# Optimization experiments

Hardware: AMD Instinct MI355X
Metric: run time of the kernel (lower is better)

The kernel has to match this reference:

```python
import jax, jax.numpy as jnp
import numpy as np

EDGES = np.array([[0,13],[0,1],[0,4],[0,10],[0,7],[13,14],[14,15],[15,16],[1,2],[2,3],
                  [3,17],[4,5],[5,6],[6,18],[10,11],[11,12],[12,19],[7,8],[8,9],[9,20]])
N = 21
EPS = 1e-5


def _build_adj():
    # adj_mx_from_edges: symmetric binary adjacency + self-loops, row-normalized (D^-1 (A+I))
    A = np.zeros((N, N), np.float32)
    A[EDGES[:, 0], EDGES[:, 1]] = 1.0
    A = np.maximum(A, A.T)
    A = A + np.eye(N, dtype=np.float32)
    A = A / A.sum(1, keepdims=True)
    return A


def setup_inputs() -> dict:
    key = jax.random.key(0)
    ks = jax.random.split(key, 10)
    B, C, H, W = 64, 256, 64, 64
    s = 0.05
    return {
        "feature_s": jax.random.normal(ks[0], (B, C, H, W), jnp.float32),
        "target_s": jax.random.uniform(ks[1], (B, N, H, W), jnp.float32),
        "adj": jnp.asarray(_build_adj()),
        "bn_gamma": jnp.ones((N,), jnp.float32),
        "bn_beta": jnp.zeros((N,), jnp.float32),
        "gru_wx": s * jax.random.normal(ks[2], (256, 768), jnp.float32),
        "gru_wh": s * jax.random.normal(ks[3], (256, 768), jnp.float32),
        "gru_bx": jnp.zeros((768,), jnp.float32),
        "gru_bh": jnp.zeros((768,), jnp.float32),
        "w_g1": s * jax.random.normal(ks[4], (2, 256, 256), jnp.float32),
        "b_g1": jnp.zeros((256,), jnp.float32),
        "w_g2": s * jax.random.normal(ks[5], (2, 256, 256), jnp.float32),
        "b_g2": jnp.zeros((256,), jnp.float32),
        "w_out": s * jax.random.normal(ks[6], (2, 256, 3), jnp.float32),
        "b_out": jnp.zeros((3,), jnp.float32),
    }


def _batchnorm1d(x, gamma, beta):
    # x: [B, 21, C]; BatchNorm1d over channel dim 21 (stats over batch and length)
    mean = jnp.mean(x, axis=(0, 2), keepdims=True)
    var = jnp.var(x, axis=(0, 2), keepdims=True)
    xn = (x - mean) * jax.lax.rsqrt(var + EPS)
    return xn * gamma[None, :, None] + beta[None, :, None]


def _gru(x, wx, wh, bx, bh):
    # standard GRU scanned over the 21-joint axis; x: [B, N, 256] -> [B, N, 256]
    B, n, Hd = x.shape
    xg = jnp.einsum('bnc,ch->bnh', x, wx) + bx  # [B, N, 3H]

    def step(h, xg_t):
        hg = h @ wh + bh
        r = jax.nn.sigmoid(xg_t[..., :Hd] + hg[..., :Hd])
        z = jax.nn.sigmoid(xg_t[..., Hd:2 * Hd] + hg[..., Hd:2 * Hd])
        ncand = jnp.tanh(xg_t[..., 2 * Hd:] + r * hg[..., 2 * Hd:])
        h_new = (1.0 - z) * ncand + z * h
        return h_new, h_new

    h0 = jnp.zeros((B, Hd), x.dtype)
    _, ys = jax.lax.scan(step, h0, jnp.swapaxes(xg, 0, 1))
    return jnp.swapaxes(ys, 0, 1)


def _laplacian(adj):
    # normalized Laplacian L = I - D^{-1/2} A D^{-1/2}
    d = adj.sum(-1)
    dinv = jnp.where(d > 0, jax.lax.rsqrt(jnp.where(d > 0, d, 1.0)), 0.0)
    return jnp.eye(N, dtype=adj.dtype) - dinv[:, None] * adj * dinv[None, :]


def _chebconv(x, L, w, b):
    # K=2 Chebyshev conv: T0 = I, T1 = L ->  x @ W0 + (L x) @ W1 + b
    return jnp.einsum('bnc,co->bno', x, w[0]) + jnp.einsum('nm,bmc,co->bno', L, x, w[1]) + b


def reference(feature_s, target_s, adj, bn_gamma, bn_beta,
              gru_wx, gru_wh, gru_bx, gru_bh,
              w_g1, b_g1, w_g2, b_g2, w_out, b_out):
    B, C, H, W = feature_s.shape
    # batched correlation: [B, 21, HW] x [B, HW, C] -> [B, 21, C]
    q = jnp.einsum('bjp,bcp->bjc',
                   target_s.reshape(B, N, H * W),
                   feature_s.reshape(B, C, H * W))
    q = _batchnorm1d(q, bn_gamma, bn_beta)
    q = jnp.where(q > 0, q, 0.1 * q)  # LeakyReLU(0.1)
    q = _gru(q, gru_wx, gru_wh, gru_bx, gru_bh)
    # _ResChebGC: two graph convs with ReLU + residual (dropout = identity in eval)
    L = _laplacian(adj)
    h = jax.nn.relu(_chebconv(q, L, w_g1, b_g1))
    h = jax.nn.relu(_chebconv(h, L, w_g2, b_g2))
    x = q + h
    return _chebconv(x, L, w_out, b_out)  # [B, 21, 3]
```

## Files before the change

### kernel.cpp

```cpp
#include <hip/hip_runtime.h>
#include <cstdint>

#define B   64
#define NJ  21
#define CHN 256
#define HW  4096
#define G3  768

typedef _Float16 f16x8 __attribute__((ext_vector_type(8)));
typedef float    f32x4 __attribute__((ext_vector_type(4)));
typedef _Float16 f16x2 __attribute__((ext_vector_type(2)));
typedef __fp16   fp16x2v __attribute__((ext_vector_type(2)));
union PKU { fp16x2v h; unsigned u; };
union HU { unsigned u; f16x2 h; };

static __device__ inline unsigned pack_f16(float a, float b){
  HU u; u.h.x = (_Float16)a; u.h.y = (_Float16)b; return u.u;
}

static __device__ inline float fdot2f(unsigned wu, unsigned hu, float acc){
  HU w, h; w.u = wu; h.u = hu;
#if __has_builtin(__builtin_amdgcn_fdot2)
  return __builtin_amdgcn_fdot2(w.h, h.h, acc, false);
#else
  return acc + (float)w.h.x*(float)h.h.x + (float)w.h.y*(float)h.h.y;
#endif
}

__global__ __launch_bounds__(64) void k_lap(const float* __restrict__ adj, float* __restrict__ L){
  __shared__ float dinv[NJ];
  int t = threadIdx.x;
  if (t < NJ){
    float s = 0.f;
    for (int j=0;j<NJ;j++) s += adj[t*NJ+j];
    dinv[t] = s > 0.f ? 1.f/sqrtf(s) : 0.f;
  }
  __syncthreads();
  for (int idx=t; idx<NJ*NJ; idx+=64){
    int i = idx/NJ, j = idx%NJ;
    L[idx] = (i==j ? 1.f : 0.f) - dinv[i]*adj[idx]*dinv[j];
  }
}

__global__ __launch_bounds__(256,4) void k_corr3(const float* __restrict__ T,
    const float* __restrict__ F, _Float16* __restrict__ P){
  int bid = blockIdx.x;
  int nb = bid & 3, b = (bid>>2)&63, kb = bid>>8;
  int t = threadIdx.x;
  int w = t>>6, l = t&63;
  __shared__ __align__(16) unsigned short At[2][32*64];
  __shared__ __align__(16) unsigned short Bt[2][64*64];

  for (int i=t; i<704; i+=256){
    int bi = (i>=352) ? 1 : 0; int r2 = i - bi*352;
    int r = 21 + (r2>>5); int kk = r2 & 31;
    *(unsigned*)((char*)&At[bi][0] + r*128 + kk*4) = 0u;
  }

  bool isF = (t < 128);
  bool isT = (t >= 128) && (t < 170);
  const float4* gp = nullptr; int srow = 0, shalf = 0;
  if (isF){
    srow = t>>1; shalf = t&1;
    gp = (const float4*)(F + ((size_t)b*CHN + nb*64 + srow)*HW + (size_t)kb*1024) + shalf*8;
  } else if (isT){
    int tt = t-128; srow = tt>>1; shalf = tt&1;
    gp = (const float4*)(T + ((size_t)b*NJ + srow)*HW + (size_t)kb*1024) + shalf*8;
  }
  float4 ld[8];
  if (gp){
    #pragma unroll
    for (int i=0;i<8;i++) ld[i] = gp[i];
  }

  f32x4 acc0 = {0.f,0.f,0.f,0.f}, acc1 = {0.f,0.f,0.f,0.f};
  int arow0 = (l&15);
  int brow  = w*16 + (l&15);
  int kbyt  = (l>>4)*16;

  for (int s=0; s<16; ++s){
    int bi = s & 1;
    if (gp){
      unsigned short* tile = isF ? &Bt[bi][0] : &At[bi][0];
      #pragma unroll
      for (int q=0;q<4;q++){
        PKU p0, p1, p2, p3;
        p0.h = __builtin_amdgcn_cvt_pkrtz(ld[2*q].x,   ld[2*q].y);
        p1.h = __builtin_amdgcn_cvt_pkrtz(ld[2*q].z,   ld[2*q].w);
        p2.h = __builtin_amdgcn_cvt_pkrtz(ld[2*q+1].x, ld[2*q+1].y);
        p3.h = __builtin_amdgcn_cvt_pkrtz(ld[2*q+1].z, ld[2*q+1].w);
        int addr = (srow*128 + shalf*64 + q*16) ^ ((srow&7)<<4);
        uint4 v; v.x = p0.u; v.y = p1.u; v.z = p2.u; v.w = p3.u;
        *(uint4*)((char*)tile + addr) = v;
      }
      if (s < 15){
        const float4* gn = gp + (size_t)(s+1)*16;
        #pragma unroll
        for (int i=0;i<8;i++) ld[i] = gn[i];
      }
    }
    asm volatile("s_waitcnt lgkmcnt(0)\n\ts_barrier" ::: "memory");
    #pragma unroll
    for (int kc=0;kc<2;kc++){
      int kb2 = kc*64 + kbyt;
      int ab0 = ((arow0)*128    + kb2) ^ ((arow0&7)<<4);
      int ab1 = ((arow0+16)*128 + kb2) ^ ((arow0&7)<<4);
      int bb  = ((brow)*128     + kb2) ^ ((brow&7)<<4);
      f16x8 a0 = *(const f16x8*)((const char*)&At[bi][0] + ab0);
      f16x8 a1 = *(const f16x8*)((const char*)&At[bi][0] + ab1);
      f16x8 bf = *(const f16x8*)((const char*)&Bt[bi][0] + bb);
      acc0 = __builtin_amdgcn_mfma_f32_16x16x32_f16(a0, bf, acc0, 0, 0, 0);
      acc1 = __builtin_amdgcn_mfma_f32_16x16x32_f16(a1, bf, acc1, 0, 0, 0);
    }
  }

  int cbase = nb*64 + w*16 + (l&15);
  #pragma unroll
  for (int r=0;r<4;r++){
    int row0 = (l>>4)*4 + r;
    if (row0 < 21)
      P[(((size_t)kb*64 + b)*21 + row0)*256 + cbase] = (_Float16)acc0[r];
    int row1 = row0 + 16;
    if (row1 < 21)
      P[(((size_t)kb*64 + b)*21 + row1)*256 + cbase] = (_Float16)acc1[r];
  }
}

__global__ __launch_bounds__(256) void k_stats(const _Float16* __restrict__ P,
    float* __restrict__ q, float* __restrict__ stats){
  int j = blockIdx.x, t = threadIdx.x;
  const size_t KSTRIDE = (size_t)64*21*256;
  float s = 0.f, ss = 0.f;
  for (int b=0;b<B;b++){
    size_t i0 = ((size_t)b*21 + j)*256 + t;
    float v = (float)P[i0] + (float)P[KSTRIDE + i0]
            + (float)P[2*KSTRIDE + i0] + (float)P[3*KSTRIDE + i0];
    q[((size_t)b*NJ + j)*CHN + t] = v;
    s += v; ss += v*v;
  }
  #pragma unroll
  for (int o=32;o>0;o>>=1){ s += __shfl_down(s,o); ss += __shfl_down(ss,o); }
  __shared__ float sb[4], ssb[4];
  int wid = t>>6;
  if ((t&63)==0){ sb[wid]=s; ssb[wid]=ss; }
  __syncthreads();
  if (t==0){
    float S  = sb[0]+sb[1]+sb[2]+sb[3];
    float SS = ssb[0]+ssb[1]+ssb[2]+ssb[3];
    float mean = S * (1.f/16384.f);
    float var  = SS * (1.f/16384.f) - mean*mean;
    stats[j]      = mean;
    stats[NJ + j] = 1.f/sqrtf(var + 1e-5f);
  }
}

__global__ __launch_bounds__(256) void k_xg(const float* __restrict__ q,
    const float* __restrict__ stats, const float* __restrict__ gamma, const float* __restrict__ beta,
    const float* __restrict__ wx, const float* __restrict__ bx, float* __restrict__ xg){
  int b = blockIdx.x/3, sl = blockIdx.x%3;
  int t = threadIdx.x;
  int col = sl*256 + t;
  __shared__ float xn[NJ][CHN];
  for (int idx=t; idx<NJ*CHN; idx+=256){
    int j = idx >> 8;
    float v = (q[(size_t)b*NJ*CHN + idx] - stats[j]) * stats[NJ+j];
    v = v * gamma[j] + beta[j];
    xn[j][idx & 255] = v > 0.f ? v : 0.1f*v;
  }
  __syncthreads();
  float acc[NJ];
  #pragma unroll
  for (int j=0;j<NJ;j++) acc[j]=0.f;
  for (int c=0;c<CHN;c++){
    float wv = wx[(size_t)c*G3 + col];
    #pragma unroll
    for (int j=0;j<NJ;j++) acc[j] += xn[j][c]*wv;
  }
  float bv = bx[col];
  #pragma unroll
  for (int j=0;j<NJ;j++) xg[((size_t)b*NJ+j)*G3 + col] = acc[j] + bv;
}

__global__ __launch_bounds__(256) void k_pack(const float* __restrict__ wh, unsigned* __restrict__ whp){
  int idx = blockIdx.x*256 + threadIdx.x;
  int c2 = idx / G3, col = idx % G3;
  float w0 = wh[(size_t)(2*c2)*G3 + col];
  float w1 = wh[(size_t)(2*c2+1)*G3 + col];
  whp[idx] = pack_f16(w0, w1);
}

__global__ __launch_bounds__(768,3) void k_gru(const unsigned* __restrict__ whp,
    const float* __restrict__ bh, const float* __restrict__ xg, float* __restrict__ gout){
  int b = blockIdx.x;
  int col = threadIdx.x;
  int l = col & 63;
  __shared__ float hf[256];
  __shared__ float lr[256], lz[256];
  unsigned wr[64];
  #pragma unroll
  for (int i=0;i<64;i++) wr[i] = whp[i*G3 + col];
  const unsigned* wsp = whp + 64*G3 + col;
  float bhv = bh[col];
  if (col < 256) hf[col] = 0.f;
  unsigned hv0 = 0u, hv1 = 0u;
  float xv_next = xg[((size_t)b*NJ + 0)*G3 + col];
  __syncthreads();
  for (int step=0; step<NJ; ++step){
    float xvc = xv_next;
    if (step < NJ-1) xv_next = xg[((size_t)b*NJ + step+1)*G3 + col];
    float a0 = 0.f, a1 = 0.f;
    #pragma unroll
    for (int i=0;i<64;i++)
      a1 = fdot2f(wsp[(size_t)i*G3], __builtin_amdgcn_readlane(hv1, i), a1);
    #pragma unroll
    for (int i=0;i<64;i++)
      a0 = fdot2f(wr[i], __builtin_amdgcn_readlane(hv0, i), a0);
    float a = a0 + a1 + bhv;
    if (col < 256)      lr[col]     = 1.f/(1.f+__expf(-(xvc + a)));
    else if (col < 512) lz[col-256] = 1.f/(1.f+__expf(-(xvc + a)));
    __syncthreads();
    if (col >= 512){
      int i = col - 512;
      float nv = tanhf(xvc + lr[i]*a);
      float z  = lz[i];
      float hnew = (1.f - z)*nv + z*hf[i];
      gout[((size_t)b*NJ + step)*CHN + i] = hnew;
      hf[i] = hnew;
    }
    __syncthreads();
    float2 p0 = *(const float2*)&hf[2*l];
    float2 p1 = *(const float2*)&hf[128 + 2*l];
    hv0 = pack_f16(p0.x, p0.y);
    hv1 = pack_f16(p1.x, p1.y);
  }
}

__global__ __launch_bounds__(256) void k_cheb(const float* __restrict__ xin,
    const float* __restrict__ Lm, const float* __restrict__ W,
    const float* __restrict__ bvec, float* __restrict__ out){
  int b = blockIdx.x >> 2, oq = blockIdx.x & 3;
  int t = threadIdx.x;
  int ol = t & 63, ck = t >> 6;
  __shared__ float xs[NJ][CHN];
  __shared__ float lx[NJ][CHN];
  __shared__ float part[4][64][NJ];
  for (int idx=t; idx<NJ*CHN; idx+=256) xs[idx>>8][idx&255] = xin[(size_t)b*NJ*CHN + idx];
  __syncthreads();
  for (int idx=t; idx<NJ*CHN; idx+=256){
    int j = idx>>8, c = idx&255;
    float sacc = 0.f;
    #pragma unroll
    for (int m=0;m<NJ;m++) sacc += Lm[j*NJ+m]*xs[m][c];
    lx[j][c] = sacc;
  }
  __syncthreads();
  int o = oq*64 + ol;
  float acc[NJ];
  #pragma unroll
  for (int j=0;j<NJ;j++) acc[j]=0.f;
  const float* W0 = W;
  const float* W1 = W + CHN*CHN;
  for (int cc=0; cc<64; ++cc){
    int c = ck*64 + cc;
    float w0 = W0[(size_t)c*CHN + o];
    float w1 = W1[(size_t)c*CHN + o];
    #pragma unroll
    for (int j=0;j<NJ;j++){ acc[j] += xs[j][c]*w0; acc[j] += lx[j][c]*w1; }
  }
  #pragma unroll
  for (int j=0;j<NJ;j++) part[ck][ol][j] = acc[j];
  __syncthreads();
  for (int idx=t; idx<64*NJ; idx+=256){
    int o2 = idx & 63, j = idx >> 6;
    float s2 = part[0][o2][j]+part[1][o2][j]+part[2][o2][j]+part[3][o2][j] + bvec[oq*64+o2];
    s2 = s2 > 0.f ? s2 : 0.f;
    out[(size_t)b*NJ*CHN + j*CHN + oq*64 + o2] = s2;
  }
}

__global__ __launch_bounds__(64) void k_out(const float* __restrict__ gq, const float* __restrict__ h2,
    const float* __restrict__ Lm, const float* __restrict__ W, const float* __restrict__ bvec,
    float* __restrict__ out){
  int b = blockIdx.x, t = threadIdx.x;
  __shared__ float xs[NJ][CHN];
  __shared__ float lx[NJ][CHN];
  for (int idx=t; idx<NJ*CHN; idx+=64)
    xs[idx>>8][idx&255] = gq[(size_t)b*NJ*CHN+idx] + h2[(size_t)b*NJ*CHN+idx];
  __syncthreads();
  for (int idx=t; idx<NJ*CHN; idx+=64){
    int j = idx>>8, c = idx&255;
    float s = 0.f;
    #pragma unroll
    for (int m=0;m<NJ;m++) s += Lm[j*NJ+m]*xs[m][c];
    lx[j][c] = s;
  }
  __syncthreads();
  if (t < 63){
    int j = t/3, o = t%3;
    float acc = bvec[o];
    const float* W0 = W;
    const float* W1 = W + CHN*3;
    for (int c=0;c<CHN;c++){
      acc += xs[j][c]*W0[c*3+o];
      acc += lx[j][c]*W1[c*3+o];
    }
    out[(size_t)b*63 + t] = acc;
  }
}

extern "C" void kernel_launch(void* const* d_in, const int* in_sizes, int n_in,
                              void* d_out, int out_size, void* d_ws, size_t ws_size,
                              hipStream_t stream){
  const float* feat  = (const float*)d_in[0];
  const float* targ  = (const float*)d_in[1];
  const float* adj   = (const float*)d_in[2];
  const float* gamma = (const float*)d_in[3];
  const float* beta  = (const float*)d_in[4];
  const float* wx    = (const float*)d_in[5];
  const float* wh    = (const float*)d_in[6];
  const float* bx    = (const float*)d_in[7];
  const float* bh    = (const float*)d_in[8];
  const float* wg1   = (const float*)d_in[9];
  const float* bg1   = (const float*)d_in[10];
  const float* wg2   = (const float*)d_in[11];
  const float* bg2   = (const float*)d_in[12];
  const float* wout  = (const float*)d_in[13];
  const float* bout  = (const float*)d_in[14];

  float* ws   = (float*)d_ws;
  float* q     = ws + 0;
  float* stats = ws + 400000;
  float* Lw    = ws + 400128;
  float* xgw   = ws + 500000;
  float* gout  = ws + 1600000;
  float* h1    = ws + 2000000;
  float* h2b   = ws + 2400000;
  unsigned* whp = (unsigned*)(ws + 2800000);
  _Float16* P  = (_Float16*)(ws + 3000000);

  k_lap  <<<1,    64, 0, stream>>>(adj, Lw);
  k_pack <<<384, 256, 0, stream>>>(wh, whp);
  k_corr3<<<1024,256, 0, stream>>>(targ, feat, P);
  k_stats<<<21,  256, 0, stream>>>(P, q, stats);
  k_xg   <<<192, 256, 0, stream>>>(q, stats, gamma, beta, wx, bx, xgw);
  k_gru  <<<64,  768, 0, stream>>>(whp, bh, xgw, gout);
  k_cheb <<<256, 256, 0, stream>>>(gout, Lw, wg1, bg1, h1);
  k_cheb <<<256, 256, 0, stream>>>(h1,   Lw, wg2, bg2, h2b);
  k_out  <<<64,   64, 0, stream>>>(gout, h2b, Lw, wout, bout, (float*)d_out);
}
```

Before: 269.6 us.

## Stage target tile once in LDS and stream features directly into MFMA registers

The correlation kernel now loads the whole 21x1024 target slice for a batch and K-split into shared memory once, converted to fp16 with a swizzled layout. Feature rows are no longer staged in LDS: each lane reads its float4 pairs straight from global memory, packs them to fp16 in registers and feeds them as the MFMA B operand. This removes the per-step double-buffered tile stores and barriers. Blocks grow to 512 threads covering 128 channels, so the grid halves. In exchange the kernel uses 64KB of LDS per block, which limits occupancy, and feature loads are only latency-hidden by the unrolled loop.

```diff
diff --git a/kernel.cpp b/kernel.cpp
--- a/kernel.cpp
+++ b/kernel.cpp
@@ -13,6 +13,7 @@
 typedef __fp16   fp16x2v __attribute__((ext_vector_type(2)));
 union PKU { fp16x2v h; unsigned u; };
 union HU { unsigned u; f16x2 h; };
+union FRU { f16x8 v; unsigned u[4]; };
 
 static __device__ inline unsigned pack_f16(float a, float b){
   HU u; u.h.x = (_Float16)a; u.h.y = (_Float16)b; return u.u;
@@ -42,87 +43,63 @@
   }
 }
 
-__global__ __launch_bounds__(256,4) void k_corr3(const float* __restrict__ T,
+__global__ __launch_bounds__(512,4) void k_corr6(const float* __restrict__ T,
     const float* __restrict__ F, _Float16* __restrict__ P){
   int bid = blockIdx.x;
-  int nb = bid & 3, b = (bid>>2)&63, kb = bid>>8;
+  int nb = bid & 1, kb = (bid>>1)&3, b = bid>>3;
   int t = threadIdx.x;
   int w = t>>6, l = t&63;
-  __shared__ __align__(16) unsigned short At[2][32*64];
-  __shared__ __align__(16) unsigned short Bt[2][64*64];
-
-  for (int i=t; i<704; i+=256){
-    int bi = (i>=352) ? 1 : 0; int r2 = i - bi*352;
-    int r = 21 + (r2>>5); int kk = r2 & 31;
-    *(unsigned*)((char*)&At[bi][0] + r*128 + kk*4) = 0u;
-  }
-
-  bool isF = (t < 128);
-  bool isT = (t >= 128) && (t < 170);
-  const float4* gp = nullptr; int srow = 0, shalf = 0;
-  if (isF){
-    srow = t>>1; shalf = t&1;
-    gp = (const float4*)(F + ((size_t)b*CHN + nb*64 + srow)*HW + (size_t)kb*1024) + shalf*8;
-  } else if (isT){
-    int tt = t-128; srow = tt>>1; shalf = tt&1;
-    gp = (const float4*)(T + ((size_t)b*NJ + srow)*HW + (size_t)kb*1024) + shalf*8;
-  }
-  float4 ld[8];
-  if (gp){
-    #pragma unroll
-    for (int i=0;i<8;i++) ld[i] = gp[i];
-  }
-
+  __shared__ __align__(16) unsigned short Tl[32*1024];
+
+  for (int i=t; i<5632; i+=512){
+    int r = 21 + (i>>9), pr = i & 511;
+    int addr = (r*2048 + pr*4) ^ ((r&7)<<4);
+    *(unsigned*)((char*)Tl + addr) = 0u;
+  }
+  {
+    const float2* Tp = (const float2*)(T + (size_t)b*NJ*HW + (size_t)kb*1024);
+    for (int i=t; i<21*512; i+=512){
+      int r = i>>9, pr = i & 511;
+      float2 v = Tp[(size_t)r*2048 + pr];
+      PKU pk; pk.h = __builtin_amdgcn_cvt_pkrtz(v.x, v.y);
+      int addr = (r*2048 + pr*4) ^ ((r&7)<<4);
+      *(unsigned*)((char*)Tl + addr) = pk.u;
+    }
+  }
+  __syncthreads();
+
+  int cl = l & 15, kg = l >> 4;
+  const float4* Fp = (const float4*)(F + ((size_t)b*CHN + nb*128 + w*16 + cl)*HW
+                                       + (size_t)kb*1024) + kg*2;
   f32x4 acc0 = {0.f,0.f,0.f,0.f}, acc1 = {0.f,0.f,0.f,0.f};
-  int arow0 = (l&15);
-  int brow  = w*16 + (l&15);
-  int kbyt  = (l>>4)*16;
-
-  for (int s=0; s<16; ++s){
-    int bi = s & 1;
-    if (gp){
-      unsigned short* tile = isF ? &Bt[bi][0] : &At[bi][0];
-      #pragma unroll
-      for (int q=0;q<4;q++){
-        PKU p0, p1, p2, p3;
-        p0.h = __builtin_amdgcn_cvt_pkrtz(ld[2*q].x,   ld[2*q].y);
-        p1.h = __builtin_amdgcn_cvt_pkrtz(ld[2*q].z,   ld[2*q].w);
-        p2.h = __builtin_amdgcn_cvt_pkrtz(ld[2*q+1].x, ld[2*q+1].y);
-        p3.h = __builtin_amdgcn_cvt_pkrtz(ld[2*q+1].z, ld[2*q+1].w);
-        int addr = (srow*128 + shalf*64 + q*16) ^ ((srow&7)<<4);
-        uint4 v; v.x = p0.u; v.y = p1.u; v.z = p2.u; v.w = p3.u;
-        *(uint4*)((char*)tile + addr) = v;
-      }
-      if (s < 15){
-        const float4* gn = gp + (size_t)(s+1)*16;
-        #pragma unroll
-        for (int i=0;i<8;i++) ld[i] = gn[i];
-      }
-    }
-    asm volatile("s_waitcnt lgkmcnt(0)\n\ts_barrier" ::: "memory");
-    #pragma unroll
-    for (int kc=0;kc<2;kc++){
-      int kb2 = kc*64 + kbyt;
-      int ab0 = ((arow0)*128    + kb2) ^ ((arow0&7)<<4);
-      int ab1 = ((arow0+16)*128 + kb2) ^ ((arow0&7)<<4);
-      int bb  = ((brow)*128     + kb2) ^ ((brow&7)<<4);
-      f16x8 a0 = *(const f16x8*)((const char*)&At[bi][0] + ab0);
-      f16x8 a1 = *(const f16x8*)((const char*)&At[bi][0] + ab1);
-      f16x8 bf = *(const f16x8*)((const char*)&Bt[bi][0] + bb);
-      acc0 = __builtin_amdgcn_mfma_f32_16x16x32_f16(a0, bf, acc0, 0, 0, 0);
-      acc1 = __builtin_amdgcn_mfma_f32_16x16x32_f16(a1, bf, acc1, 0, 0, 0);
-    }
-  }
-
-  int cbase = nb*64 + w*16 + (l&15);
-  #pragma unroll
-  for (int r=0;r<4;r++){
-    int row0 = (l>>4)*4 + r;
+  int r = l & 15;
+  int swz = (r&7)<<4;
+
+  #pragma unroll 4
+  for (int chunk=0; chunk<32; ++chunk){
+    float4 f0 = Fp[chunk*8];
+    float4 f1 = Fp[chunk*8 + 1];
+    FRU bf;
+    bf.u[0] = pack_f16(f0.x, f0.y);
+    bf.u[1] = pack_f16(f0.z, f0.w);
+    bf.u[2] = pack_f16(f1.x, f1.y);
+    bf.u[3] = pack_f16(f1.z, f1.w);
+    int kbyte = chunk*64 + kg*16;
+    f16x8 a0 = *(const f16x8*)((const char*)Tl + ((r*2048      + kbyte) ^ swz));
+    f16x8 a1 = *(const f16x8*)((const char*)Tl + (((r+16)*2048 + kbyte) ^ swz));
+    acc0 = __builtin_amdgcn_mfma_f32_16x16x32_f16(a0, bf.v, acc0, 0, 0, 0);
+    acc1 = __builtin_amdgcn_mfma_f32_16x16x32_f16(a1, bf.v, acc1, 0, 0, 0);
+  }
+
+  int cbase = nb*128 + w*16 + (l&15);
+  #pragma unroll
+  for (int i=0;i<4;i++){
+    int row0 = (l>>4)*4 + i;
     if (row0 < 21)
-      P[(((size_t)kb*64 + b)*21 + row0)*256 + cbase] = (_Float16)acc0[r];
+      P[(((size_t)kb*64 + b)*21 + row0)*256 + cbase] = (_Float16)acc0[i];
     int row1 = row0 + 16;
     if (row1 < 21)
-      P[(((size_t)kb*64 + b)*21 + row1)*256 + cbase] = (_Float16)acc1[r];
+      P[(((size_t)kb*64 + b)*21 + row1)*256 + cbase] = (_Float16)acc1[i];
   }
 }
 
@@ -340,7 +317,7 @@
 
   k_lap  <<<1,    64, 0, stream>>>(adj, Lw);
   k_pack <<<384, 256, 0, stream>>>(wh, whp);
-  k_corr3<<<1024,256, 0, stream>>>(targ, feat, P);
+  k_corr6<<<512, 512, 0, stream>>>(targ, feat, P);
   k_stats<<<21,  256, 0, stream>>>(P, q, stats);
   k_xg   <<<192, 256, 0, stream>>>(q, stats, gamma, beta, wx, bx, xgw);
   k_gru  <<<64,  768, 0, stream>>>(whp, bh, xgw, gout);
```

Measured after the change: 262.3 us. 1.03x faster.
